# Optimization experiments

Measured on AMD Instinct MI355X. Metric: run time of the kernel, lower is better.

## Reference

```python
import jax, jax.numpy as jnp
import numpy as np

N, C, H, W = 2, 128, 128, 128
GROUP, K, PAD, STRIDE, DIL = 4, 3, 1, 1, 1
DW = 3
GC = C // GROUP
P = K * K
OFFSET_SCALE = 1.0
LN_EPS = 1e-6


def setup_inputs() -> dict:
    key = jax.random.key(0)
    ks = jax.random.split(key, 8)
    inp = jax.random.normal(ks[0], (N, C, H, W), jnp.float32)
    x = jax.random.normal(ks[1], (N, H, W, C), jnp.float32)
    dw_w = jax.random.normal(ks[2], (DW, DW, 1, C), jnp.float32) * 0.1   # HWIO depthwise
    dw_b = jax.random.normal(ks[3], (C,), jnp.float32) * 0.1
    ln_g = jnp.ones((C,), jnp.float32)
    ln_b = jnp.zeros((C,), jnp.float32)
    off_w = jax.random.normal(ks[4], (GROUP * P * 2, C), jnp.float32) * 0.01
    off_b = jax.random.normal(ks[5], (GROUP * P * 2,), jnp.float32) * 0.01
    return dict(input=inp, x=x, dw_w=dw_w, dw_b=dw_b, ln_g=ln_g, ln_b=ln_b,
                off_w=off_w, off_b=off_b)


def _dw_branch(inp, dw_w, dw_b, ln_g, ln_b):
    # depthwise conv (groups=C) -> LayerNorm (channels_last) -> GELU
    y = jax.lax.conv_general_dilated(
        inp, dw_w, window_strides=(1, 1), padding=[(PAD * 0 + (DW - 1) // 2,) * 2] * 2,
        dimension_numbers=('NCHW', 'HWIO', 'NCHW'), feature_group_count=C)
    y = y + dw_b[None, :, None, None]
    y = jnp.transpose(y, (0, 2, 3, 1))  # NHWC
    mu = y.mean(-1, keepdims=True)
    var = y.var(-1, keepdims=True)
    y = (y - mu) * jax.lax.rsqrt(var + LN_EPS) * ln_g + ln_b
    return jax.nn.gelu(y, approximate=False)


def _dcnv3(x, offset):
    # x: [N,H,W,C] channels_last; offset: [N,H,W,GROUP*P*2]; mask is all-ones.
    xp = jnp.pad(x, ((0, 0), (PAD, PAD), (PAD, PAD), (0, 0)))
    Hin, Win = H + 2 * PAD, W + 2 * PAD
    base = (DIL * (K - 1)) // 2
    ref_y = (base + 0.5 + jnp.arange(H, dtype=jnp.float32) * STRIDE) / Hin
    ref_x = (base + 0.5 + jnp.arange(W, dtype=jnp.float32) * STRIDE) / Win
    RX, RY = jnp.meshgrid(ref_x, ref_y)            # [H,W] each, RX varies with w
    ref = jnp.stack([RX, RY], -1)                  # [H,W,2] (x,y) normalized
    pts = (-base + jnp.arange(K, dtype=jnp.float32) * DIL)
    PX, PY = jnp.meshgrid(pts, pts, indexing='ij')  # x outer, y inner (torch order)
    grid = jnp.stack([PX, PY], -1).reshape(P, 2) / jnp.array([Win, Hin], jnp.float32)
    off = offset.reshape(N, H, W, GROUP, P, 2)
    loc = (ref[None, :, :, None, None, :]
           + grid[None, None, None, None, :, :] * OFFSET_SCALE
           + off * OFFSET_SCALE / jnp.array([Win, Hin], jnp.float32))
    # grid_sample, align_corners=False: pixel = loc*size - 0.5
    ix = loc[..., 0] * Win - 0.5
    iy = loc[..., 1] * Hin - 0.5
    x0 = jnp.floor(ix)
    y0 = jnp.floor(iy)
    wx = ix - x0
    wy = iy - y0
    x0i = x0.astype(jnp.int32)
    y0i = y0.astype(jnp.int32)
    xg = xp.reshape(N, Hin * Win, GROUP, GC).transpose(0, 2, 1, 3)  # [N,G,HinWin,gc]

    def flat(a):  # [N,H,W,G,P] -> [N,G,H*W*P]
        return a.transpose(0, 3, 1, 2, 4).reshape(N, GROUP, H * W * P)

    def gather(yy, xx):
        valid = (yy >= 0) & (yy < Hin) & (xx >= 0) & (xx < Win)
        idx = jnp.clip(yy, 0, Hin - 1) * Win + jnp.clip(xx, 0, Win - 1)
        v = jnp.take_along_axis(xg, flat(idx)[..., None], axis=2)  # [N,G,L,gc]
        return v * flat(valid).astype(xg.dtype)[..., None]

    out = (gather(y0i, x0i) * flat((1 - wy) * (1 - wx))[..., None]
           + gather(y0i, x0i + 1) * flat((1 - wy) * wx)[..., None]
           + gather(y0i + 1, x0i) * flat(wy * (1 - wx))[..., None]
           + gather(y0i + 1, x0i + 1) * flat(wy * wx)[..., None])
    out = out.reshape(N, GROUP, H * W, P, GC).sum(3)               # mask == 1
    out = out.reshape(N, GROUP, H, W, GC).transpose(0, 2, 3, 1, 4).reshape(N, H, W, C)
    return out


def reference(input, x, dw_w, dw_b, ln_g, ln_b, off_w, off_b):
    x1 = _dw_branch(input, dw_w, dw_b, ln_g, ln_b)          # [N,H,W,C]
    offset = jnp.einsum('nhwc,oc->nhwo', x1, off_w) + off_b  # [N,H,W,G*P*2]
    out = _dcnv3(x, offset)                                  # [N,H,W,C]
    return jnp.transpose(out, (0, 3, 1, 2))                  # NCHW
```

## Files before the change

### kernel.cpp

```cpp
#include <hip/hip_runtime.h>
#include <hip/hip_fp16.h>
#include <math.h>

#define N_  2
#define C_  128
#define H_  128
#define W_  128
#define G_  4
#define GC_ 32
#define P_  9
#define X1S 132

union HU { __half h; unsigned short u; };
static __device__ __forceinline__ unsigned int f2h(float f) {
    HU x; x.h = __float2half(f); return (unsigned int)x.u;
}
static __device__ __forceinline__ float h2f(unsigned int v) {
    HU x; x.u = (unsigned short)v; return __half2float(x.h);
}
static __device__ __forceinline__ unsigned short f2bf(float f) {
    unsigned int u = __float_as_uint(f);
    u += 0x7FFFu + ((u >> 16) & 1u);
    return (unsigned short)(u >> 16);
}
static __device__ __forceinline__ float bflo(unsigned int u) {
    return __uint_as_float(u << 16);
}
static __device__ __forceinline__ float bfhi(unsigned int u) {
    return __uint_as_float(u & 0xFFFF0000u);
}

static __device__ __forceinline__ float erf_fast(float x) {
    const float ax = fabsf(x);
    const float t  = __builtin_amdgcn_rcpf(fmaf(0.3275911f, ax, 1.0f));
    float p = fmaf(1.061405429f, t, -1.453152027f);
    p = fmaf(p, t, 1.421413741f);
    p = fmaf(p, t, -0.284496736f);
    p = fmaf(p, t, 0.254829592f);
    p = p * t;
    const float e = __expf(-ax * ax);
    const float y = fmaf(-p, e, 1.0f);
    return copysignf(y, x);
}

using bf16x8 = __attribute__((ext_vector_type(8))) short;
using f32x4  = __attribute__((ext_vector_type(4))) float;

#define K_X1T   0
#define K_STAT  4480
#define K_OFFS  13056
#define K_RED1  18432
#define K_RED2  18688
#define K_OFFW  18944
#define K_ARENA 38528

__global__ __launch_bounds__(256, 4)
void dcn_fused(const float* __restrict__ inp,
               const float* __restrict__ xin,
               const float* __restrict__ dww,
               const float* __restrict__ dwb,
               const float* __restrict__ lng,
               const float* __restrict__ lnb,
               const float* __restrict__ offw,
               const float* __restrict__ offb,
               float* __restrict__ out)
{
    __shared__ __align__(16) char arena[K_ARENA];
    unsigned short* inb   = (unsigned short*)arena;
    unsigned short* x1t   = (unsigned short*)(arena + K_X1T);
    float*          stat  = (float*)(arena + K_STAT);
    float*          offs  = (float*)(arena + K_OFFS);
    float*          stage = (float*)arena;
    float* red1 = (float*)(arena + K_RED1);
    float* red2 = (float*)(arena + K_RED2);
    unsigned short* offwt = (unsigned short*)(arena + K_OFFW);
    uint4* desc_lds = (uint4*)(arena + K_OFFW);

    const int t   = threadIdx.x;
    const int bid = blockIdx.x;
    const int sw  = ((bid & 7) << 8) | (bid >> 3);
    const int wq  = sw & 7;
    const int h   = (sw >> 3) & (H_ - 1);
    const int n   = sw >> 10;
    const int w0  = wq * 16;

    {
        #pragma unroll
        for (int k = 0; k < 9; ++k) {
            const int q   = t + 256 * k;
            const int seg = q / 6;
            const int i   = q - seg * 6;
            const int c   = seg / 3;
            const int r   = seg - c * 3;
            const int hr  = h - 1 + r;
            const int col0 = w0 - 4 + 4 * i;
            float4 v = make_float4(0.f, 0.f, 0.f, 0.f);
            if (hr >= 0 && hr < H_ && col0 >= 0 && col0 <= W_ - 4)
                v = *(const float4*)&inp[(((size_t)n * C_ + c) * H_ + hr) * W_ + col0];
            *(ushort4*)&inb[seg * 24 + 4 * i] =
                make_ushort4(f2bf(v.x), f2bf(v.y), f2bf(v.z), f2bf(v.w));
        }
        const float4* src = (const float4*)offw;
        #pragma unroll
        for (int k = 0; k < 9; ++k) {
            const int i = t + 256 * k;
            const int o = i >> 5;
            const int u = i & 31;
            const float4 v = src[i];
            *(ushort4*)&offwt[o * 136 + u * 4] =
                make_ushort4(f2bf(v.x), f2bf(v.y), f2bf(v.z), f2bf(v.w));
        }
    }
    __syncthreads();

    const int pq = t & 3;
    const int cg = t >> 2;
    const int c0 = cg * 2;
    float acc[2][4];
    {
        const float2 bias = *(const float2*)&dwb[c0];
        #pragma unroll
        for (int j = 0; j < 4; ++j) { acc[0][j] = bias.x; acc[1][j] = bias.y; }
        #pragma unroll
        for (int r = 0; r < 3; ++r) {
            const float2 wd0 = *(const float2*)&dww[(r * 3 + 0) * C_ + c0];
            const float2 wd1 = *(const float2*)&dww[(r * 3 + 1) * C_ + c0];
            const float2 wd2 = *(const float2*)&dww[(r * 3 + 2) * C_ + c0];
            #pragma unroll
            for (int ch = 0; ch < 2; ++ch) {
                const int seg = (c0 + ch) * 3 + r;
                const unsigned short* rp = &inb[seg * 24 + 4 * pq];
                const uint2 a = *(const uint2*)rp;
                const uint2 b = *(const uint2*)(rp + 4);
                const unsigned int s8 = rp[8];
                const float v3 = bfhi(a.y);
                const float v4 = bflo(b.x);
                const float v5 = bfhi(b.x);
                const float v6 = bflo(b.y);
                const float v7 = bfhi(b.y);
                const float v8 = bflo(s8);
                const float k0 = ch ? wd0.y : wd0.x;
                const float k1 = ch ? wd1.y : wd1.x;
                const float k2 = ch ? wd2.y : wd2.x;
                acc[ch][0] = fmaf(v3, k0, acc[ch][0]);
                acc[ch][0] = fmaf(v4, k1, acc[ch][0]);
                acc[ch][0] = fmaf(v5, k2, acc[ch][0]);
                acc[ch][1] = fmaf(v4, k0, acc[ch][1]);
                acc[ch][1] = fmaf(v5, k1, acc[ch][1]);
                acc[ch][1] = fmaf(v6, k2, acc[ch][1]);
                acc[ch][2] = fmaf(v5, k0, acc[ch][2]);
                acc[ch][2] = fmaf(v6, k1, acc[ch][2]);
                acc[ch][2] = fmaf(v7, k2, acc[ch][2]);
                acc[ch][3] = fmaf(v6, k0, acc[ch][3]);
                acc[ch][3] = fmaf(v7, k1, acc[ch][3]);
                acc[ch][3] = fmaf(v8, k2, acc[ch][3]);
            }
        }
    }

    {
        float s1[4], s2[4];
        #pragma unroll
        for (int j = 0; j < 4; ++j) {
            s1[j] = acc[0][j] + acc[1][j];
            s2[j] = fmaf(acc[1][j], acc[1][j], acc[0][j] * acc[0][j]);
        }
        #pragma unroll
        for (int m = 4; m <= 32; m <<= 1) {
            #pragma unroll
            for (int j = 0; j < 4; ++j) {
                s1[j] += __shfl_xor(s1[j], m);
                s2[j] += __shfl_xor(s2[j], m);
            }
        }
        const int lane = t & 63;
        const int wave = t >> 6;
        if ((lane >> 2) == 0) {
            #pragma unroll
            for (int j = 0; j < 4; ++j) {
                red1[wave * 16 + 4 * pq + j] = s1[j];
                red2[wave * 16 + 4 * pq + j] = s2[j];
            }
        }
    }
    __syncthreads();
    if (t < 16) {
        float s1 = 0.f, s2 = 0.f;
        #pragma unroll
        for (int w = 0; w < 4; ++w) { s1 += red1[w * 16 + t]; s2 += red2[w * 16 + t]; }
        const float mean = s1 * (1.f / 128.f);
        const float var  = s2 * (1.f / 128.f) - mean * mean;
        stat[t]      = mean;
        stat[16 + t] = rsqrtf(var + 1e-6f);
    }
    __syncthreads();

    {
        const float2 lg = *(const float2*)&lng[c0];
        const float2 lb = *(const float2*)&lnb[c0];
        #pragma unroll
        for (int j = 0; j < 4; ++j) {
            const int px = 4 * pq + j;
            const float mean = stat[px];
            const float rstd = stat[16 + px];
            float v0 = (acc[0][j] - mean) * rstd * lg.x + lb.x;
            float v1 = (acc[1][j] - mean) * rstd * lg.y + lb.y;
            v0 = 0.5f * v0 * (1.f + erf_fast(v0 * 0.70710678118654752440f));
            v1 = 0.5f * v1 * (1.f + erf_fast(v1 * 0.70710678118654752440f));
            *(ushort2*)&x1t[px * 136 + c0] = make_ushort2(f2bf(v0), f2bf(v1));
        }
    }
    __syncthreads();

    {
        const int lane = t & 63;
        const int wave = t >> 6;
        const int m16  = lane & 15;
        const int kb   = lane >> 4;
        bf16x8 afr[4];
        #pragma unroll
        for (int st = 0; st < 4; ++st)
            afr[st] = *(const bf16x8*)&x1t[m16 * 136 + st * 32 + kb * 8];
        #pragma unroll
        for (int pass = 0; pass < 2; ++pass) {
            const int nt = (pass == 0) ? wave : 4;
            if (pass == 1 && wave != 0) break;
            const int orow = nt * 16 + m16;
            const bool ov = (orow < 72);
            const int orc = ov ? orow : 0;
            const bf16x8 b0 = *(const bf16x8*)&offwt[orc * 136 + 0 * 32 + kb * 8];
            const bf16x8 b1 = *(const bf16x8*)&offwt[orc * 136 + 1 * 32 + kb * 8];
            const bf16x8 b2 = *(const bf16x8*)&offwt[orc * 136 + 2 * 32 + kb * 8];
            const bf16x8 b3 = *(const bf16x8*)&offwt[orc * 136 + 3 * 32 + kb * 8];
            const float bias = ov ? offb[orow] : 0.f;
            f32x4 a4 = {bias, bias, bias, bias};
            a4 = __builtin_amdgcn_mfma_f32_16x16x32_bf16(afr[0], b0, a4, 0, 0, 0);
            a4 = __builtin_amdgcn_mfma_f32_16x16x32_bf16(afr[1], b1, a4, 0, 0, 0);
            a4 = __builtin_amdgcn_mfma_f32_16x16x32_bf16(afr[2], b2, a4, 0, 0, 0);
            a4 = __builtin_amdgcn_mfma_f32_16x16x32_bf16(afr[3], b3, a4, 0, 0, 0);
            if (ov) {
                #pragma unroll
                for (int reg = 0; reg < 4; ++reg) {
                    const int pxl = kb * 4 + reg;
                    offs[pxl * 76 + orow] = a4[reg];
                }
            }
        }
    }
    __syncthreads();

    for (int tap = t; tap < 16 * 36; tap += 256) {
        const int pix = tap / 36;
        const int rem = tap - pix * 36;
        const int g   = rem / 9;
        const int p   = rem - g * 9;
        const float ox = offs[pix * 76 + g * 18 + 2 * p];
        const float oy = offs[pix * 76 + g * 18 + 2 * p + 1];
        const float fy = (float)(h + (p % 3)) + oy;
        const float fx = (float)(w0 + pix + (p / 3)) + ox;
        const float y0f = floorf(fy);
        const float x0f = floorf(fx);
        const float wy = fy - y0f;
        const float wx = fx - x0f;
        const int y0 = (int)y0f;
        const int x0 = (int)x0f;
        const int yc0 = min(max(y0, 1), H_) - 1;
        const int yc1 = min(max(y0 + 1, 1), H_) - 1;
        const int xc0 = min(max(x0, 1), W_) - 1;
        const int xc1 = min(max(x0 + 1, 1), W_) - 1;
        const float a0 = (1.f - wy) * ((y0 >= 1 && y0 <= H_) ? 1.f : 0.f);
        const float a1 = wy * ((y0 + 1 >= 1 && y0 + 1 <= H_) ? 1.f : 0.f);
        const float b0 = (1.f - wx) * ((x0 >= 1 && x0 <= W_) ? 1.f : 0.f);
        const float b1 = wx * ((x0 + 1 >= 1 && x0 + 1 <= W_) ? 1.f : 0.f);
        const unsigned int i00 = (unsigned int)(yc0 * W_ + xc0);
        const unsigned int i01 = (unsigned int)(yc0 * W_ + xc1);
        const unsigned int i10 = (unsigned int)(yc1 * W_ + xc0);
        const unsigned int i11 = (unsigned int)(yc1 * W_ + xc1);
        desc_lds[tap] = make_uint4(i00 | (i01 << 16),
                                   i10 | (i11 << 16),
                                   f2h(a0 * b0) | (f2h(a0 * b1) << 16),
                                   f2h(a1 * b0) | (f2h(a1 * b1) << 16));
    }
    __syncthreads();

    {
        const int k  = t & 7;
        const int pl = t >> 3;
        const float4* xb = (const float4*)xin + (size_t)n * (H_ * W_ * (C_ / 4)) + k;
        #pragma unroll
        for (int it = 0; it < 2; ++it) {
            const int pair = it * 32 + pl;
            const int pix  = pair >> 2;
            const int g    = pair & 3;
            const uint4* dp = desc_lds + pair * 9;
            const float4* xg = xb + g * (GC_ / 4);
            uint4 d[9];
            #pragma unroll
            for (int p = 0; p < P_; ++p) d[p] = dp[p];
            float4 a4 = make_float4(0.f, 0.f, 0.f, 0.f);
            #pragma unroll
            for (int p = 0; p < P_; ++p) {
                const float4 v00 = xg[(d[p].x & 0xFFFFu) * 32u];
                const float4 v01 = xg[(d[p].x >> 16) * 32u];
                const float4 v10 = xg[(d[p].y & 0xFFFFu) * 32u];
                const float4 v11 = xg[(d[p].y >> 16) * 32u];
                const float w00 = h2f(d[p].z & 0xFFFFu), w01 = h2f(d[p].z >> 16);
                const float w10 = h2f(d[p].w & 0xFFFFu), w11 = h2f(d[p].w >> 16);
                a4.x = fmaf(w00, v00.x, a4.x);
                a4.y = fmaf(w00, v00.y, a4.y);
                a4.z = fmaf(w00, v00.z, a4.z);
                a4.w = fmaf(w00, v00.w, a4.w);
                a4.x = fmaf(w01, v01.x, a4.x);
                a4.y = fmaf(w01, v01.y, a4.y);
                a4.z = fmaf(w01, v01.z, a4.z);
                a4.w = fmaf(w01, v01.w, a4.w);
                a4.x = fmaf(w10, v10.x, a4.x);
                a4.y = fmaf(w10, v10.y, a4.y);
                a4.z = fmaf(w10, v10.z, a4.z);
                a4.w = fmaf(w10, v10.w, a4.w);
                a4.x = fmaf(w11, v11.x, a4.x);
                a4.y = fmaf(w11, v11.y, a4.y);
                a4.z = fmaf(w11, v11.z, a4.z);
                a4.w = fmaf(w11, v11.w, a4.w);
            }
            *(float4*)&stage[pix * X1S + g * GC_ + k * 4] = a4;
        }
    }
    __syncthreads();

    {
        const int pix = t & 15;
        const int cq  = t >> 4;
        #pragma unroll
        for (int i = 0; i < 8; ++i) {
            const int c = cq + 16 * i;
            out[(((size_t)n * C_ + c) * H_ + h) * W_ + w0 + pix] = stage[pix * X1S + c];
        }
    }
}

extern "C" void kernel_launch(void* const* d_in, const int* in_sizes, int n_in,
                              void* d_out, int out_size, void* d_ws, size_t ws_size,
                              hipStream_t stream) {
    const float* inp  = (const float*)d_in[0];
    const float* xin  = (const float*)d_in[1];
    const float* dww  = (const float*)d_in[2];
    const float* dwb  = (const float*)d_in[3];
    const float* lng  = (const float*)d_in[4];
    const float* lnb  = (const float*)d_in[5];
    const float* offw = (const float*)d_in[6];
    const float* offb = (const float*)d_in[7];
    float* outp = (float*)d_out;

    dcn_fused<<<dim3(2048), dim3(256), 0, stream>>>(
        inp, xin, dww, dwb, lng, lnb, offw, offb, outp);
}
```

Measured before the change: 41.12 us.

## Double block size to 512 threads and halve per-thread work in each stage

The fused kernel now launches 512 threads per block instead of 256, with every stage re-partitioned to match. The depthwise conv gives each thread 2 pixels instead of 4, the LayerNorm reduction spans 8 waves, 5 waves each run one MFMA tile for the offset GEMM, and each thread handles one bilinear gather pair instead of two. The aim is more parallelism and memory-level parallelism per block for the latency-bound gather phase. In exchange it adds guarded loops, idle waves in the GEMM stage, and higher per-block register and LDS pressure that may reduce the number of resident blocks.

```diff
diff --git a/kernel.cpp b/kernel.cpp
--- a/kernel.cpp
+++ b/kernel.cpp
@@ -50,11 +50,11 @@
 #define K_STAT  4480
 #define K_OFFS  13056
 #define K_RED1  18432
-#define K_RED2  18688
-#define K_OFFW  18944
-#define K_ARENA 38528
-
-__global__ __launch_bounds__(256, 4)
+#define K_RED2  18944
+#define K_OFFW  19456
+#define K_ARENA 39040
+
+__global__ __launch_bounds__(512, 4)
 void dcn_fused(const float* __restrict__ inp,
                const float* __restrict__ xin,
                const float* __restrict__ dww,
@@ -86,41 +86,45 @@
 
     {
         #pragma unroll
-        for (int k = 0; k < 9; ++k) {
-            const int q   = t + 256 * k;
-            const int seg = q / 6;
-            const int i   = q - seg * 6;
-            const int c   = seg / 3;
-            const int r   = seg - c * 3;
-            const int hr  = h - 1 + r;
-            const int col0 = w0 - 4 + 4 * i;
-            float4 v = make_float4(0.f, 0.f, 0.f, 0.f);
-            if (hr >= 0 && hr < H_ && col0 >= 0 && col0 <= W_ - 4)
-                v = *(const float4*)&inp[(((size_t)n * C_ + c) * H_ + hr) * W_ + col0];
-            *(ushort4*)&inb[seg * 24 + 4 * i] =
-                make_ushort4(f2bf(v.x), f2bf(v.y), f2bf(v.z), f2bf(v.w));
+        for (int k = 0; k < 5; ++k) {
+            const int q = t + 512 * k;
+            if (q < 2304) {
+                const int seg = q / 6;
+                const int i   = q - seg * 6;
+                const int c   = seg / 3;
+                const int r   = seg - c * 3;
+                const int hr  = h - 1 + r;
+                const int col0 = w0 - 4 + 4 * i;
+                float4 v = make_float4(0.f, 0.f, 0.f, 0.f);
+                if (hr >= 0 && hr < H_ && col0 >= 0 && col0 <= W_ - 4)
+                    v = *(const float4*)&inp[(((size_t)n * C_ + c) * H_ + hr) * W_ + col0];
+                *(ushort4*)&inb[seg * 24 + 4 * i] =
+                    make_ushort4(f2bf(v.x), f2bf(v.y), f2bf(v.z), f2bf(v.w));
+            }
         }
         const float4* src = (const float4*)offw;
         #pragma unroll
-        for (int k = 0; k < 9; ++k) {
-            const int i = t + 256 * k;
-            const int o = i >> 5;
-            const int u = i & 31;
-            const float4 v = src[i];
-            *(ushort4*)&offwt[o * 136 + u * 4] =
-                make_ushort4(f2bf(v.x), f2bf(v.y), f2bf(v.z), f2bf(v.w));
-        }
-    }
-    __syncthreads();
-
-    const int pq = t & 3;
-    const int cg = t >> 2;
+        for (int k = 0; k < 5; ++k) {
+            const int i = t + 512 * k;
+            if (i < 2304) {
+                const int o = i >> 5;
+                const int u = i & 31;
+                const float4 v = src[i];
+                *(ushort4*)&offwt[o * 136 + u * 4] =
+                    make_ushort4(f2bf(v.x), f2bf(v.y), f2bf(v.z), f2bf(v.w));
+            }
+        }
+    }
+    __syncthreads();
+
+    const int pq = t & 7;
+    const int cg = t >> 3;
     const int c0 = cg * 2;
-    float acc[2][4];
+    float acc[2][2];
     {
         const float2 bias = *(const float2*)&dwb[c0];
-        #pragma unroll
-        for (int j = 0; j < 4; ++j) { acc[0][j] = bias.x; acc[1][j] = bias.y; }
+        acc[0][0] = bias.x; acc[0][1] = bias.x;
+        acc[1][0] = bias.y; acc[1][1] = bias.y;
         #pragma unroll
         for (int r = 0; r < 3; ++r) {
             const float2 wd0 = *(const float2*)&dww[(r * 3 + 0) * C_ + c0];
@@ -129,57 +133,48 @@
             #pragma unroll
             for (int ch = 0; ch < 2; ++ch) {
                 const int seg = (c0 + ch) * 3 + r;
-                const unsigned short* rp = &inb[seg * 24 + 4 * pq];
+                const unsigned short* rp = &inb[seg * 24 + 2 * pq + 2];
                 const uint2 a = *(const uint2*)rp;
-                const uint2 b = *(const uint2*)(rp + 4);
-                const unsigned int s8 = rp[8];
-                const float v3 = bfhi(a.y);
-                const float v4 = bflo(b.x);
-                const float v5 = bfhi(b.x);
-                const float v6 = bflo(b.y);
-                const float v7 = bfhi(b.y);
-                const float v8 = bflo(s8);
+                const unsigned int s4 = rp[4];
+                const float va = bfhi(a.x);
+                const float vb = bflo(a.y);
+                const float vc = bfhi(a.y);
+                const float vd = bflo(s4);
                 const float k0 = ch ? wd0.y : wd0.x;
                 const float k1 = ch ? wd1.y : wd1.x;
                 const float k2 = ch ? wd2.y : wd2.x;
-                acc[ch][0] = fmaf(v3, k0, acc[ch][0]);
-                acc[ch][0] = fmaf(v4, k1, acc[ch][0]);
-                acc[ch][0] = fmaf(v5, k2, acc[ch][0]);
-                acc[ch][1] = fmaf(v4, k0, acc[ch][1]);
-                acc[ch][1] = fmaf(v5, k1, acc[ch][1]);
-                acc[ch][1] = fmaf(v6, k2, acc[ch][1]);
-                acc[ch][2] = fmaf(v5, k0, acc[ch][2]);
-                acc[ch][2] = fmaf(v6, k1, acc[ch][2]);
-                acc[ch][2] = fmaf(v7, k2, acc[ch][2]);
-                acc[ch][3] = fmaf(v6, k0, acc[ch][3]);
-                acc[ch][3] = fmaf(v7, k1, acc[ch][3]);
-                acc[ch][3] = fmaf(v8, k2, acc[ch][3]);
-            }
-        }
-    }
-
-    {
-        float s1[4], s2[4];
-        #pragma unroll
-        for (int j = 0; j < 4; ++j) {
+                acc[ch][0] = fmaf(va, k0, acc[ch][0]);
+                acc[ch][0] = fmaf(vb, k1, acc[ch][0]);
+                acc[ch][0] = fmaf(vc, k2, acc[ch][0]);
+                acc[ch][1] = fmaf(vb, k0, acc[ch][1]);
+                acc[ch][1] = fmaf(vc, k1, acc[ch][1]);
+                acc[ch][1] = fmaf(vd, k2, acc[ch][1]);
+            }
+        }
+    }
+
+    {
+        float s1[2], s2[2];
+        #pragma unroll
+        for (int j = 0; j < 2; ++j) {
             s1[j] = acc[0][j] + acc[1][j];
             s2[j] = fmaf(acc[1][j], acc[1][j], acc[0][j] * acc[0][j]);
         }
         #pragma unroll
-        for (int m = 4; m <= 32; m <<= 1) {
+        for (int m = 8; m <= 32; m <<= 1) {
             #pragma unroll
-            for (int j = 0; j < 4; ++j) {
+            for (int j = 0; j < 2; ++j) {
                 s1[j] += __shfl_xor(s1[j], m);
                 s2[j] += __shfl_xor(s2[j], m);
             }
         }
         const int lane = t & 63;
         const int wave = t >> 6;
-        if ((lane >> 2) == 0) {
+        if ((lane >> 3) == 0) {
             #pragma unroll
-            for (int j = 0; j < 4; ++j) {
-                red1[wave * 16 + 4 * pq + j] = s1[j];
-                red2[wave * 16 + 4 * pq + j] = s2[j];
+            for (int j = 0; j < 2; ++j) {
+                red1[wave * 16 + 2 * pq + j] = s1[j];
+                red2[wave * 16 + 2 * pq + j] = s2[j];
             }
         }
     }
@@ -187,7 +182,7 @@
     if (t < 16) {
         float s1 = 0.f, s2 = 0.f;
         #pragma unroll
-        for (int w = 0; w < 4; ++w) { s1 += red1[w * 16 + t]; s2 += red2[w * 16 + t]; }
+        for (int w = 0; w < 8; ++w) { s1 += red1[w * 16 + t]; s2 += red2[w * 16 + t]; }
         const float mean = s1 * (1.f / 128.f);
         const float var  = s2 * (1.f / 128.f) - mean * mean;
         stat[t]      = mean;
@@ -199,8 +194,8 @@
         const float2 lg = *(const float2*)&lng[c0];
         const float2 lb = *(const float2*)&lnb[c0];
         #pragma unroll
-        for (int j = 0; j < 4; ++j) {
-            const int px = 4 * pq + j;
+        for (int j = 0; j < 2; ++j) {
+            const int px = 2 * pq + j;
             const float mean = stat[px];
             const float rstd = stat[16 + px];
             float v0 = (acc[0][j] - mean) * rstd * lg.x + lb.x;
@@ -215,17 +210,14 @@
     {
         const int lane = t & 63;
         const int wave = t >> 6;
-        const int m16  = lane & 15;
-        const int kb   = lane >> 4;
-        bf16x8 afr[4];
-        #pragma unroll
-        for (int st = 0; st < 4; ++st)
-            afr[st] = *(const bf16x8*)&x1t[m16 * 136 + st * 32 + kb * 8];
-        #pragma unroll
-        for (int pass = 0; pass < 2; ++pass) {
-            const int nt = (pass == 0) ? wave : 4;
-            if (pass == 1 && wave != 0) break;
-            const int orow = nt * 16 + m16;
+        if (wave < 5) {
+            const int m16 = lane & 15;
+            const int kb  = lane >> 4;
+            bf16x8 afr[4];
+            #pragma unroll
+            for (int st = 0; st < 4; ++st)
+                afr[st] = *(const bf16x8*)&x1t[m16 * 136 + st * 32 + kb * 8];
+            const int orow = wave * 16 + m16;
             const bool ov = (orow < 72);
             const int orc = ov ? orow : 0;
             const bf16x8 b0 = *(const bf16x8*)&offwt[orc * 136 + 0 * 32 + kb * 8];
@@ -249,7 +241,7 @@
     }
     __syncthreads();
 
-    for (int tap = t; tap < 16 * 36; tap += 256) {
+    for (int tap = t; tap < 16 * 36; tap += 512) {
         const int pix = tap / 36;
         const int rem = tap - pix * 36;
         const int g   = rem / 9;
@@ -284,47 +276,43 @@
     __syncthreads();
 
     {
-        const int k  = t & 7;
-        const int pl = t >> 3;
-        const float4* xb = (const float4*)xin + (size_t)n * (H_ * W_ * (C_ / 4)) + k;
-        #pragma unroll
-        for (int it = 0; it < 2; ++it) {
-            const int pair = it * 32 + pl;
-            const int pix  = pair >> 2;
-            const int g    = pair & 3;
-            const uint4* dp = desc_lds + pair * 9;
-            const float4* xg = xb + g * (GC_ / 4);
-            uint4 d[9];
-            #pragma unroll
-            for (int p = 0; p < P_; ++p) d[p] = dp[p];
-            float4 a4 = make_float4(0.f, 0.f, 0.f, 0.f);
-            #pragma unroll
-            for (int p = 0; p < P_; ++p) {
-                const float4 v00 = xg[(d[p].x & 0xFFFFu) * 32u];
-                const float4 v01 = xg[(d[p].x >> 16) * 32u];
-                const float4 v10 = xg[(d[p].y & 0xFFFFu) * 32u];
-                const float4 v11 = xg[(d[p].y >> 16) * 32u];
-                const float w00 = h2f(d[p].z & 0xFFFFu), w01 = h2f(d[p].z >> 16);
-                const float w10 = h2f(d[p].w & 0xFFFFu), w11 = h2f(d[p].w >> 16);
-                a4.x = fmaf(w00, v00.x, a4.x);
-                a4.y = fmaf(w00, v00.y, a4.y);
-                a4.z = fmaf(w00, v00.z, a4.z);
-                a4.w = fmaf(w00, v00.w, a4.w);
-                a4.x = fmaf(w01, v01.x, a4.x);
-                a4.y = fmaf(w01, v01.y, a4.y);
-                a4.z = fmaf(w01, v01.z, a4.z);
-                a4.w = fmaf(w01, v01.w, a4.w);
-                a4.x = fmaf(w10, v10.x, a4.x);
-                a4.y = fmaf(w10, v10.y, a4.y);
-                a4.z = fmaf(w10, v10.z, a4.z);
-                a4.w = fmaf(w10, v10.w, a4.w);
-                a4.x = fmaf(w11, v11.x, a4.x);
-                a4.y = fmaf(w11, v11.y, a4.y);
-                a4.z = fmaf(w11, v11.z, a4.z);
-                a4.w = fmaf(w11, v11.w, a4.w);
-            }
-            *(float4*)&stage[pix * X1S + g * GC_ + k * 4] = a4;
-        }
+        const int k    = t & 7;
+        const int pair = t >> 3;
+        const int pix  = pair >> 2;
+        const int g    = pair & 3;
+        const uint4* dp = desc_lds + pair * 9;
+        const float4* xg = (const float4*)xin
+            + (size_t)n * (H_ * W_ * (C_ / 4)) + g * (GC_ / 4) + k;
+        uint4 d[9];
+        #pragma unroll
+        for (int p = 0; p < P_; ++p) d[p] = dp[p];
+        float4 a4 = make_float4(0.f, 0.f, 0.f, 0.f);
+        #pragma unroll
+        for (int p = 0; p < P_; ++p) {
+            const float4 v00 = xg[(d[p].x & 0xFFFFu) * 32u];
+            const float4 v01 = xg[(d[p].x >> 16) * 32u];
+            const float4 v10 = xg[(d[p].y & 0xFFFFu) * 32u];
+            const float4 v11 = xg[(d[p].y >> 16) * 32u];
+            const float w00 = h2f(d[p].z & 0xFFFFu), w01 = h2f(d[p].z >> 16);
+            const float w10 = h2f(d[p].w & 0xFFFFu), w11 = h2f(d[p].w >> 16);
+            a4.x = fmaf(w00, v00.x, a4.x);
+            a4.y = fmaf(w00, v00.y, a4.y);
+            a4.z = fmaf(w00, v00.z, a4.z);
+            a4.w = fmaf(w00, v00.w, a4.w);
+            a4.x = fmaf(w01, v01.x, a4.x);
+            a4.y = fmaf(w01, v01.y, a4.y);
+            a4.z = fmaf(w01, v01.z, a4.z);
+            a4.w = fmaf(w01, v01.w, a4.w);
+            a4.x = fmaf(w10, v10.x, a4.x);
+            a4.y = fmaf(w10, v10.y, a4.y);
+            a4.z = fmaf(w10, v10.z, a4.z);
+            a4.w = fmaf(w10, v10.w, a4.w);
+            a4.x = fmaf(w11, v11.x, a4.x);
+            a4.y = fmaf(w11, v11.y, a4.y);
+            a4.z = fmaf(w11, v11.z, a4.z);
+            a4.w = fmaf(w11, v11.w, a4.w);
+        }
+        *(float4*)&stage[pix * X1S + g * GC_ + k * 4] = a4;
     }
     __syncthreads();
 
@@ -332,8 +320,8 @@
         const int pix = t & 15;
         const int cq  = t >> 4;
         #pragma unroll
-        for (int i = 0; i < 8; ++i) {
-            const int c = cq + 16 * i;
+        for (int i = 0; i < 4; ++i) {
+            const int c = cq + 32 * i;
             out[(((size_t)n * C_ + c) * H_ + h) * W_ + w0 + pix] = stage[pix * X1S + c];
         }
     }
@@ -352,6 +340,6 @@
     const float* offb = (const float*)d_in[7];
     float* outp = (float*)d_out;
 
-    dcn_fused<<<dim3(2048), dim3(256), 0, stream>>>(
+    dcn_fused<<<dim3(2048), dim3(512), 0, stream>>>(
         inp, xin, dww, dwb, lng, lnb, offw, offb, outp);
 }
```

Result: slower. 48.92 us (+19.0%).
